# Optimization experiments

Hardware: AMD Instinct MI355X
Metric: run time of the kernel (lower is better)

The kernel has to match this reference:

```python
import jax, jax.numpy as jnp
import numpy as np

N = 100000
INC = 128
GRID = 256
S = 2  # scale s for voxel_to_aux coarse pooling


def _ln(x, g, b, eps=1e-6):
    m = jnp.mean(x, axis=-1, keepdims=True)
    v = jnp.var(x, axis=-1, keepdims=True)
    return (x - m) / jnp.sqrt(v + eps) * g + b


def setup_inputs() -> dict:
    rng = np.random.default_rng(0)
    lin = rng.choice(GRID ** 3, size=N, replace=False)
    x = (lin // (GRID * GRID)).astype(np.int64)
    y = ((lin // GRID) % GRID).astype(np.int64)
    z = (lin % GRID).astype(np.int64)
    coords = np.stack([x, y, z], axis=1).astype(np.int32)
    # sparse 3x3x3 neighbor table (pad index = N for missing neighbors)
    order = np.argsort(lin)
    lin_sorted = lin[order]
    nbr_idx = np.full((N, 27), N, dtype=np.int32)
    k = 0
    for dx in (-1, 0, 1):
        for dy in (-1, 0, 1):
            for dz in (-1, 0, 1):
                nx, ny, nz = x + dx, y + dy, z + dz
                valid = (nx >= 0) & (nx < GRID) & (ny >= 0) & (ny < GRID) & (nz >= 0) & (nz < GRID)
                nlin = (nx * GRID + ny) * GRID + nz
                pos = np.clip(np.searchsorted(lin_sorted, nlin), 0, N - 1)
                found = valid & (lin_sorted[pos] == nlin)
                nbr_idx[:, k] = np.where(found, order[pos].astype(np.int32), N)
                k += 1
    # voxel_to_aux: coarse voxel id at scale S; counts per coarse voxel
    G2 = GRID // S
    clin = ((x // S) * G2 + (y // S)) * G2 + (z // S)
    uniq, aux_idx, counts = np.unique(clin, return_inverse=True, return_counts=True)
    counts_v = counts[aux_idx].astype(np.float32)
    num_aux = int(len(uniq))

    key = jax.random.key(0)
    ks = jax.random.split(key, 6)
    sd = 1.0 / np.sqrt(INC)
    return {
        "F": jax.random.normal(ks[0], (N, INC), jnp.float32),
        "coords": jnp.asarray(coords),
        "nbr_idx": jnp.asarray(nbr_idx),
        "aux_idx": jnp.asarray(aux_idx.astype(np.int32)),
        "counts_v": jnp.asarray(counts_v),
        "num_aux": num_aux,
        "alpha": jnp.ones((1, INC), jnp.float32),
        "w_pos": jax.random.normal(ks[1], (INC, 3), jnp.float32) * (1.0 / np.sqrt(3.0)),
        "w_pre": jax.random.normal(ks[2], (INC, INC), jnp.float32) * sd,
        "g_pre": jnp.ones((INC,), jnp.float32),
        "b_pre": jnp.zeros((INC,), jnp.float32),
        "w_conv": jax.random.normal(ks[3], (27, INC, INC), jnp.float32) * (sd / np.sqrt(27.0)),
        "g_local": jnp.ones((INC,), jnp.float32),
        "b_local": jnp.zeros((INC,), jnp.float32),
        "g_norm": jnp.ones((INC,), jnp.float32),
        "b_norm": jnp.zeros((INC,), jnp.float32),
    }


def reference(F, coords, nbr_idx, aux_idx, counts_v, num_aux, alpha, w_pos, w_pre,
              g_pre, b_pre, w_conv, g_local, b_local, g_norm, b_norm):
    inc = F.shape[1]
    # pre_mix: Linear (no bias) + LayerNorm
    F_input = _ln(F @ w_pre.T, g_pre, b_pre)
    # local_mix: sparse 3x3x3 conv on ORIGINAL features via neighbor gather
    Fp = jnp.concatenate([F, jnp.zeros((1, inc), F.dtype)], axis=0)
    gathered = Fp[nbr_idx]                               # [N, 27, inc]
    local = jnp.einsum('nkc,kcd->nd', gathered, w_conv)  # [N, inc]
    # cos_x positional reweighting
    pos = (coords.astype(jnp.float32) @ w_pos.T) * alpha  # [N, inc]
    psin, pcos = jnp.sin(pos), jnp.cos(pos)
    cat = jnp.concatenate([F_input * pcos, F_input * psin, F_input * pos], axis=1)  # [N, 3*inc]
    # voxel_to_aux (sum pool per coarse voxel) + aux_to_voxel (mean broadcast back)
    aux = jax.ops.segment_sum(cat, aux_idx, num_segments=num_aux)
    vox = aux[aux_idx] / counts_v[:, None]
    new = (vox[:, :inc] * pcos + vox[:, inc:2 * inc] * psin
           + (vox[:, 2 * inc:] - F_input * pos))
    new = _ln(new, g_norm, b_norm)
    local = _ln(local, g_local, b_local)
    return jax.nn.relu(new + local)
```

## Files before the change

### kernel.cpp

```cpp
#include <hip/hip_runtime.h>
#include <hip/hip_bf16.h>
#include <stdint.h>

#define N_PTS 100000
#define INC 128
#define NSLOT 27
#define CAPP 8192

typedef float f32x4 __attribute__((ext_vector_type(4)));
typedef short bf16x8 __attribute__((ext_vector_type(8)));

static const size_t OFF_WP   = 0;
static const size_t SZ_WP    = (size_t)NSLOT * INC * INC * 2;
static const size_t OFF_WPRE = (OFF_WP + SZ_WP + 255) & ~(size_t)255;
static const size_t SZ_WPRE  = (size_t)INC * INC * 2;
static const size_t OFF_FIN  = (OFF_WPRE + SZ_WPRE + 255) & ~(size_t)255;
static const size_t SZ_FIN   = (size_t)N_PTS * INC * 2;
static const size_t OFF_LOC  = (OFF_FIN + SZ_FIN + 255) & ~(size_t)255;
static const size_t SZ_LOC   = (size_t)N_PTS * INC * 4;
static const size_t OFF_LOC2 = (OFF_LOC + SZ_LOC + 255) & ~(size_t)255;
static const size_t SZ_LOC2  = (size_t)N_PTS * INC * 4;
static const size_t OFF_CNT  = (OFF_LOC2 + SZ_LOC2 + 255) & ~(size_t)255;
static const size_t SZ_CNT   = 128;
static const size_t OFF_DST  = (OFF_CNT + SZ_CNT + 255) & ~(size_t)255;
static const size_t SZ_DST   = (size_t)26 * CAPP * 4;
static const size_t OFF_SRC  = (OFF_DST + SZ_DST + 255) & ~(size_t)255;
static const size_t SZ_SRC   = (size_t)26 * CAPP * 4;
static const size_t OFF_FLG  = (OFF_SRC + SZ_SRC + 255) & ~(size_t)255;
static const size_t SZ_FLG   = (size_t)N_PTS;
static const size_t OFF_NDL  = (OFF_FLG + SZ_FLG + 255) & ~(size_t)255;
static const size_t SZ_NDL   = (size_t)N_PTS * 4;

#define PREP_BLOCKS 1792
#define SCAN_BLOCKS 391
#define MT64 1563
#define PAIRB 256

__device__ __forceinline__ float compute_pos3(float w0, float w1, float w2, float a,
                                              float cx, float cy, float cz) {
    return (cx * w0 + cy * w1 + cz * w2) * a;
}

__device__ __forceinline__ bf16x8 ld_cvt8(const float* __restrict__ p) {
    const float4 u = *(const float4*)p;
    const float4 v = *(const float4*)(p + 4);
    bf16x8 r;
    __hip_bfloat16* h = (__hip_bfloat16*)&r;
    h[0] = __float2bfloat16(u.x); h[1] = __float2bfloat16(u.y);
    h[2] = __float2bfloat16(u.z); h[3] = __float2bfloat16(u.w);
    h[4] = __float2bfloat16(v.x); h[5] = __float2bfloat16(v.y);
    h[6] = __float2bfloat16(v.z); h[7] = __float2bfloat16(v.w);
    return r;
}

__global__ __launch_bounds__(256) void k_front(
        const float* __restrict__ w_pre, const float* __restrict__ w_conv,
        __hip_bfloat16* __restrict__ Wp, __hip_bfloat16* __restrict__ Wpre,
        const int* __restrict__ nbr_idx, const float* __restrict__ counts_v,
        int* __restrict__ cnt, int* __restrict__ dst, int* __restrict__ src,
        unsigned char* __restrict__ flg, int* __restrict__ ndl,
        float* __restrict__ loc2) {
    __shared__ unsigned long long s_msk[4][26];
    __shared__ unsigned long long s_ndm[4];
    __shared__ int s_base[26];
    __shared__ int s_nbase;

    const int tid = threadIdx.x;

    if (blockIdx.x < PREP_BLOCKS) {
        int i = blockIdx.x * 256 + tid;
        if (i < 16384) {
            int d = i >> 7, c = i & 127;
            int j = ((c >> 5) << 12) | ((d >> 4) << 9)
                  | (((((c >> 3) & 3) << 4) + (d & 15)) << 3) | (c & 7);
            Wpre[j] = __float2bfloat16(w_pre[i]);
        } else if (i < 16384 + NSLOT * 16384) {
            int t = i - 16384;
            int slot = t >> 14, rem = t & 16383;
            int c = rem >> 7, d = rem & 127;
            int j = (slot << 14) | ((c >> 5) << 12) | ((d >> 4) << 9)
                  | (((((c >> 3) & 3) << 4) + (d & 15)) << 3) | (c & 7);
            Wp[j] = __float2bfloat16(w_conv[t]);
        }
        return;
    }

    const int w = tid >> 6, lane = tid & 63;
    const int p = (blockIdx.x - PREP_BLOCKS) * 256 + tid;
    const bool vp = p < N_PTS;

    float cv = vp ? counts_v[p] : 0.f;
    bool multi = cv > 1.5f;

    const int* nb = nbr_idx + (size_t)p * NSLOT;
    int nbr_r[NSLOT];
#pragma unroll
    for (int k = 0; k < NSLOT; ++k) nbr_r[k] = vp ? nb[k] : N_PTS;

    bool hn = false;
#pragma unroll
    for (int k = 0; k < NSLOT; ++k) {
        if (k == 13) continue;
        bool valid = nbr_r[k] < N_PTS;
        hn = hn || valid;
        unsigned long long msk = __ballot(valid);
        int b = k < 13 ? k : k - 1;
        if (lane == 0) s_msk[w][b] = msk;
    }
    bool ndv = vp && (hn || multi);
    unsigned long long ndm = __ballot(ndv);
    if (lane == 0) s_ndm[w] = ndm;
    __syncthreads();

    if (tid < 26) {
        int tot = 0;
#pragma unroll
        for (int ww = 0; ww < 4; ++ww) tot += __popcll(s_msk[ww][tid]);
        s_base[tid] = tot ? atomicAdd(&cnt[tid], tot) : 0;
    } else if (tid == 32) {
        int tot = 0;
#pragma unroll
        for (int ww = 0; ww < 4; ++ww) tot += __popcll(s_ndm[ww]);
        s_nbase = tot ? atomicAdd(&cnt[26], tot) : 0;
    }
    __syncthreads();

#pragma unroll
    for (int k = 0; k < NSLOT; ++k) {
        if (k == 13) continue;
        int b = k < 13 ? k : k - 1;
        if (nbr_r[k] < N_PTS) {
            unsigned long long msk = s_msk[w][b];
            int pre = 0;
            for (int ww = 0; ww < w; ++ww) pre += __popcll(s_msk[ww][b]);
            int gi = s_base[b] + pre + __popcll(msk & ((1ull << lane) - 1ull));
            if (gi < CAPP) { dst[b * CAPP + gi] = p; src[b * CAPP + gi] = nbr_r[k]; }
        }
    }

    if (vp) flg[p] = (unsigned char)(ndv ? 1 : 0);
    if (ndv) {
        float4* row = (float4*)(loc2 + (size_t)p * INC);
#pragma unroll
        for (int i = 0; i < INC / 4; ++i) row[i] = make_float4(0.f, 0.f, 0.f, 0.f);
        unsigned long long m2 = s_ndm[w];
        int pre = 0;
        for (int ww = 0; ww < w; ++ww) pre += __popcll(s_ndm[ww]);
        ndl[s_nbase + pre + __popcll(m2 & ((1ull << lane) - 1ull))] = p;
    }
}

__global__ __launch_bounds__(256, 3) void k_main(
        const float* __restrict__ F, const __hip_bfloat16* __restrict__ Wpre,
        const __hip_bfloat16* __restrict__ Wp, const unsigned char* __restrict__ flg,
        const float* __restrict__ g_pre, const float* __restrict__ b_pre,
        const float* __restrict__ g_local, const float* __restrict__ b_local,
        const float* __restrict__ g_norm, const float* __restrict__ b_norm,
        const int* __restrict__ cnt, const int* __restrict__ dst,
        const int* __restrict__ src,
        __hip_bfloat16* __restrict__ F_input, float* __restrict__ loc,
        float* __restrict__ loc2, float* __restrict__ outp) {
    __shared__ __hip_bfloat16 s_bf[4][16 * 136];
    __shared__ float s_gp[INC], s_bp[INC], s_gl[INC], s_bl[INC], s_gn[INC], s_bn[INC];
    __shared__ int s_wre[27], s_cntb[26];

    const int tid = threadIdx.x, w = tid >> 6, lane = tid & 63;
    const int q = lane >> 4, l15 = lane & 15;

    if (blockIdx.x >= MT64) {
        const int pb = blockIdx.x - MT64;
        if (tid < 26) { int v = cnt[tid]; if (v > CAPP) v = CAPP; s_cntb[tid] = v; }
        __syncthreads();
        if (tid == 0) {
            int accw = 0; s_wre[0] = 0;
            for (int b = 0; b < 26; ++b) { accw += (s_cntb[b] + 15) >> 4; s_wre[b + 1] = accw; }
        }
        __syncthreads();
        const int W = s_wre[26];
#pragma unroll 1
        for (int wvi = pb * 4 + w; wvi < W; wvi += PAIRB * 4) {
            int b = 0;
            while (wvi >= s_wre[b + 1]) ++b;
            int base = (wvi - s_wre[b]) << 4;
            int nB = s_cntb[b];
            int slot = b < 13 ? b : b + 1;
            const int* srcb = src + b * CAPP;
            const int* dstb = dst + b * CAPP;
            int mrow = (base + l15 < nB) ? srcb[base + l15] : 0;
            const bf16x8* Bp = (const bf16x8*)Wp + (size_t)slot * 2048;

            f32x4 acc[8];
#pragma unroll
            for (int j = 0; j < 8; ++j) acc[j] = (f32x4){0.f, 0.f, 0.f, 0.f};
#pragma unroll
            for (int ks = 0; ks < 4; ++ks) {
                bf16x8 a2 = ld_cvt8(F + (size_t)mrow * INC + ks * 32 + q * 8);
#pragma unroll
                for (int j = 0; j < 8; ++j)
                    acc[j] = __builtin_amdgcn_mfma_f32_16x16x32_bf16(
                        a2, Bp[(ks * 8 + j) * 64 + lane], acc[j], 0, 0, 0);
            }
#pragma unroll
            for (int r = 0; r < 4; ++r) {
                int m = (q << 2) + r;
                int ri = base + m;
                if (ri < nB) {
                    int d = dstb[ri];
                    float* lp = loc2 + (size_t)d * INC + l15;
#pragma unroll
                    for (int j = 0; j < 8; ++j) atomicAdd(lp + (j << 4), acc[j][r]);
                }
            }
        }
        return;
    }

    const int p0 = blockIdx.x * 64;

    if (tid < INC) {
        s_gp[tid] = g_pre[tid];   s_bp[tid] = b_pre[tid];
        s_gl[tid] = g_local[tid]; s_bl[tid] = b_local[tid];
        s_gn[tid] = g_norm[tid];  s_bn[tid] = b_norm[tid];
    }
    __syncthreads();

    int grow = p0 + (w << 4) + l15;
    if (grow >= N_PTS) grow = N_PTS - 1;

    const float* A = F + (size_t)grow * INC + q * 8;

    unsigned int fe = *(const unsigned int*)(flg + p0 + (w << 4) + (q << 2));
    unsigned char fs0 = flg[p0 + (w << 4) + q];
    unsigned char fs1 = flg[p0 + (w << 4) + 4 + q];
    unsigned char fs2 = flg[p0 + (w << 4) + 8 + q];
    unsigned char fs3 = flg[p0 + (w << 4) + 12 + q];

    bf16x8 a[4];
#pragma unroll
    for (int ks = 0; ks < 4; ++ks) a[ks] = ld_cvt8(A + ks * 32);

    const bf16x8* BP = (const bf16x8*)Wpre;
    const bf16x8* BL = (const bf16x8*)Wp + (size_t)13 * 2048;
    f32x4 accP[8], accL[8];
#pragma unroll
    for (int j = 0; j < 8; ++j) {
        accP[j] = (f32x4){0.f, 0.f, 0.f, 0.f};
        accL[j] = (f32x4){0.f, 0.f, 0.f, 0.f};
    }
    bf16x8 bP[8], bL[8];
#pragma unroll
    for (int j = 0; j < 8; ++j) bP[j] = BP[j * 64 + lane];
#pragma unroll
    for (int ks = 0; ks < 4; ++ks) {
#pragma unroll
        for (int j = 0; j < 8; ++j) bL[j] = BL[(ks * 8 + j) * 64 + lane];
#pragma unroll
        for (int j = 0; j < 8; ++j)
            accP[j] = __builtin_amdgcn_mfma_f32_16x16x32_bf16(a[ks], bP[j], accP[j], 0, 0, 0);
        if (ks < 3) {
#pragma unroll
            for (int j = 0; j < 8; ++j) bP[j] = BP[((ks + 1) * 8 + j) * 64 + lane];
        }
#pragma unroll
        for (int j = 0; j < 8; ++j)
            accL[j] = __builtin_amdgcn_mfma_f32_16x16x32_bf16(a[ks], bL[j], accL[j], 0, 0, 0);
    }

    __hip_bfloat16* sb = s_bf[w];
#pragma unroll
    for (int r = 0; r < 4; ++r) {
        int ri = (q << 2) + r;
        int p = p0 + (w << 4) + ri;
        int fl = (p < N_PTS) ? (int)((fe >> (r * 8)) & 1) : 1;

        float s = 0.f, ss = 0.f;
#pragma unroll
        for (int j = 0; j < 8; ++j) { float v = accP[j][r]; s += v; ss += v * v; }
#pragma unroll
        for (int m = 1; m < 16; m <<= 1) { s += __shfl_xor(s, m); ss += __shfl_xor(ss, m); }
        float mean = s * (1.f / 128.f);
        float rstd = rsqrtf(ss * (1.f / 128.f) - mean * mean + 1e-6f);

        float fj[8], sN = 0.f, ssN = 0.f, sL = 0.f, ssL = 0.f;
#pragma unroll
        for (int j = 0; j < 8; ++j) {
            int c = (j << 4) + l15;
            float fi = (accP[j][r] - mean) * rstd * s_gp[c] + s_bp[c];
            __hip_bfloat16 fb = __float2bfloat16(fi);
            sb[ri * 136 + c] = fb;
            float f = __bfloat162float(fb);
            fj[j] = f; sN += f; ssN += f * f;
            float v = accL[j][r]; sL += v; ssL += v * v;
        }
#pragma unroll
        for (int m = 1; m < 16; m <<= 1) {
            sN += __shfl_xor(sN, m); ssN += __shfl_xor(ssN, m);
            sL += __shfl_xor(sL, m); ssL += __shfl_xor(ssL, m);
        }
        float meanN = sN * (1.f / 128.f);
        float rstdN = rsqrtf(ssN * (1.f / 128.f) - meanN * meanN + 1e-6f);
        float meanL = sL * (1.f / 128.f);
        float rstdL = rsqrtf(ssL * (1.f / 128.f) - meanL * meanL + 1e-6f);

        if (p < N_PTS) {
            float* dp = fl ? (loc + (size_t)p * INC) : (outp + (size_t)p * INC);
#pragma unroll
            for (int j = 0; j < 8; ++j) {
                int c = (j << 4) + l15;
                float lvj = accL[j][r];
                float nn = (fj[j] - meanN) * rstdN * s_gn[c] + s_bn[c];
                float ll = (lvj - meanL) * rstdL * s_gl[c] + s_bl[c];
                float o = nn + ll; o = o > 0.f ? o : 0.f;
                dp[c] = fl ? lvj : o;
            }
        }
    }

    unsigned char fsv[4] = {fs0, fs1, fs2, fs3};
#pragma unroll
    for (int t = 0; t < 4; ++t) {
        int row = (t << 2) + q;
        int p = p0 + (w << 4) + row;
        if (p < N_PTS && (fsv[t] & 1)) {
            bf16x8 v = *(const bf16x8*)&sb[row * 136 + l15 * 8];
            *(bf16x8*)(F_input + (size_t)p * INC + l15 * 8) = v;
        }
    }
}

__global__ __launch_bounds__(256) void k_final(
        const __hip_bfloat16* __restrict__ F_input, const float* __restrict__ loc,
        const float* __restrict__ loc2,
        const int* __restrict__ nbr_idx, const int* __restrict__ coords,
        const float* __restrict__ counts_v,
        const float* __restrict__ w_pos, const float* __restrict__ alpha,
        const float* __restrict__ g_local, const float* __restrict__ b_local,
        const float* __restrict__ g_norm, const float* __restrict__ b_norm,
        const int* __restrict__ cnt, const int* __restrict__ ndl,
        float* __restrict__ out) {
    const int tid = threadIdx.x, g = tid >> 4, l15 = tid & 15;
    const int c0 = l15 * 8;
    const int nd = cnt[26];
    if (blockIdx.x * 16 >= nd) return;

    float wpv[24], pa[8], gl[8], bl[8], gn[8], bn[8];
#pragma unroll
    for (int t = 0; t < 6; ++t) ((float4*)wpv)[t] = ((const float4*)(w_pos + c0 * 3))[t];
#pragma unroll
    for (int t = 0; t < 2; ++t) {
        ((float4*)pa)[t] = ((const float4*)(alpha   + c0))[t];
        ((float4*)gl)[t] = ((const float4*)(g_local + c0))[t];
        ((float4*)bl)[t] = ((const float4*)(b_local + c0))[t];
        ((float4*)gn)[t] = ((const float4*)(g_norm  + c0))[t];
        ((float4*)bn)[t] = ((const float4*)(b_norm  + c0))[t];
    }

    for (int base = blockIdx.x * 16; base < nd; base += gridDim.x * 16) {
        int idx = base + g;
        if (idx >= nd) continue;
        int p = ndl[idx];

        float lv[8], s = 0.f, ss = 0.f;
        float4 la0 = *(const float4*)(loc  + (size_t)p * INC + c0);
        float4 la1 = *(const float4*)(loc  + (size_t)p * INC + c0 + 4);
        float4 lb0 = *(const float4*)(loc2 + (size_t)p * INC + c0);
        float4 lb1 = *(const float4*)(loc2 + (size_t)p * INC + c0 + 4);
        lv[0] = la0.x + lb0.x; lv[1] = la0.y + lb0.y;
        lv[2] = la0.z + lb0.z; lv[3] = la0.w + lb0.w;
        lv[4] = la1.x + lb1.x; lv[5] = la1.y + lb1.y;
        lv[6] = la1.z + lb1.z; lv[7] = la1.w + lb1.w;
#pragma unroll
        for (int j = 0; j < 8; ++j) { s += lv[j]; ss += lv[j] * lv[j]; }
#pragma unroll
        for (int m = 1; m < 16; m <<= 1) { s += __shfl_xor(s, m); ss += __shfl_xor(ss, m); }
        float meanL = s * (1.f / 128.f);
        float rstdL = rsqrtf(ss * (1.f / 128.f) - meanL * meanL + 1e-6f);

        float cv = counts_v[p];
        bool multi = cv > 1.5f;
        int ix = coords[p * 3 + 0], iy = coords[p * 3 + 1], iz = coords[p * 3 + 2];
        float cx = (float)ix, cy = (float)iy, cz = (float)iz;

        bf16x8 fbv = *(const bf16x8*)(F_input + (size_t)p * INC + c0);

        float psO[8], snO[8], csO[8], fO[8];
#pragma unroll
        for (int j = 0; j < 8; ++j) {
            fO[j] = __bfloat162float(((__hip_bfloat16*)&fbv)[j]);
            psO[j] = compute_pos3(wpv[j * 3], wpv[j * 3 + 1], wpv[j * 3 + 2], pa[j], cx, cy, cz);
            snO[j] = __sinf(psO[j]); csO[j] = __cosf(psO[j]);
        }

        float v0[8], v1[8], v2[8];
        if (multi) {
            float invc = 1.f / cv;
            int ox = (ix & 1) ? -1 : 1, oy = (iy & 1) ? -1 : 1, oz = (iz & 1) ? -1 : 1;
            const int* nb = nbr_idx + (size_t)p * NSLOT;
            unsigned vmask = 1u;
            bf16x8 fmv8[8];
            fmv8[0] = fbv;
#pragma unroll
            for (int e = 1; e < 8; ++e) {
                int dx = (e & 4) ? ox : 0, dy = (e & 2) ? oy : 0, dz = (e & 1) ? oz : 0;
                int m = nb[(dx + 1) * 9 + (dy + 1) * 3 + (dz + 1)];
                bool ok = m < N_PTS;
                if (ok) vmask |= (1u << e);
                int mc = ok ? m : p;
                fmv8[e] = *(const bf16x8*)(F_input + (size_t)mc * INC + c0);
            }
#pragma unroll
            for (int j = 0; j < 8; ++j) { v0[j] = 0.f; v1[j] = 0.f; v2[j] = 0.f; }
#pragma unroll
            for (int e = 0; e < 8; ++e) {
                float wt = ((vmask >> e) & 1u) ? 1.f : 0.f;
                int dx = (e & 4) ? ox : 0, dy = (e & 2) ? oy : 0, dz = (e & 1) ? oz : 0;
                float mx = cx + (float)dx, my = cy + (float)dy, mz = cz + (float)dz;
#pragma unroll
                for (int j = 0; j < 8; ++j) {
                    float fm = wt * __bfloat162float(((__hip_bfloat16*)&fmv8[e])[j]);
                    float ps = compute_pos3(wpv[j * 3], wpv[j * 3 + 1], wpv[j * 3 + 2], pa[j],
                                            mx, my, mz);
                    v0[j] += fm * __cosf(ps);
                    v1[j] += fm * __sinf(ps);
                    v2[j] += fm * ps;
                }
            }
#pragma unroll
            for (int j = 0; j < 8; ++j) { v0[j] *= invc; v1[j] *= invc; v2[j] *= invc; }
        } else {
#pragma unroll
            for (int j = 0; j < 8; ++j) {
                v0[j] = fO[j] * csO[j]; v1[j] = fO[j] * snO[j]; v2[j] = fO[j] * psO[j];
            }
        }

        float nv[8], s2 = 0.f, ss2 = 0.f;
#pragma unroll
        for (int j = 0; j < 8; ++j) {
            float nw = v0[j] * csO[j] + v1[j] * snO[j] + v2[j] - fO[j] * psO[j];
            nv[j] = nw; s2 += nw; ss2 += nw * nw;
        }
#pragma unroll
        for (int m = 1; m < 16; m <<= 1) { s2 += __shfl_xor(s2, m); ss2 += __shfl_xor(ss2, m); }
        float meanN = s2 * (1.f / 128.f);
        float rstdN = rsqrtf(ss2 * (1.f / 128.f) - meanN * meanN + 1e-6f);
        float ov[8];
#pragma unroll
        for (int j = 0; j < 8; ++j) {
            float nn = (nv[j] - meanN) * rstdN * gn[j] + bn[j];
            float ll = (lv[j] - meanL) * rstdL * gl[j] + bl[j];
            float o = nn + ll;
            ov[j] = o > 0.f ? o : 0.f;
        }
        float4* op = (float4*)(out + (size_t)p * INC + c0);
        op[0] = ((float4*)ov)[0];
        op[1] = ((float4*)ov)[1];
    }
}

extern "C" void kernel_launch(void* const* d_in, const int* in_sizes, int n_in,
                              void* d_out, int out_size, void* d_ws, size_t ws_size,
                              hipStream_t stream) {
    (void)in_sizes; (void)n_in; (void)out_size; (void)ws_size;
    const float* F        = (const float*)d_in[0];
    const int*   coords   = (const int*)d_in[1];
    const int*   nbr      = (const int*)d_in[2];
    const float* counts_v = (const float*)d_in[4];
    const float* alpha    = (const float*)d_in[6];
    const float* w_pos    = (const float*)d_in[7];
    const float* w_pre    = (const float*)d_in[8];
    const float* g_pre    = (const float*)d_in[9];
    const float* b_pre    = (const float*)d_in[10];
    const float* w_conv   = (const float*)d_in[11];
    const float* g_local  = (const float*)d_in[12];
    const float* b_local  = (const float*)d_in[13];
    const float* g_norm   = (const float*)d_in[14];
    const float* b_norm   = (const float*)d_in[15];
    float* out = (float*)d_out;

    char* ws = (char*)d_ws;
    __hip_bfloat16* Wp      = (__hip_bfloat16*)(ws + OFF_WP);
    __hip_bfloat16* Wpre    = (__hip_bfloat16*)(ws + OFF_WPRE);
    __hip_bfloat16* F_input = (__hip_bfloat16*)(ws + OFF_FIN);
    float*          loc     = (float*)(ws + OFF_LOC);
    float*          loc2    = (float*)(ws + OFF_LOC2);
    int*            cnt     = (int*)(ws + OFF_CNT);
    int*            dstb    = (int*)(ws + OFF_DST);
    int*            srcb    = (int*)(ws + OFF_SRC);
    unsigned char*  flg     = (unsigned char*)(ws + OFF_FLG);
    int*            ndl     = (int*)(ws + OFF_NDL);

    hipMemsetAsync(cnt, 0, SZ_CNT, stream);
    k_front<<<PREP_BLOCKS + SCAN_BLOCKS, 256, 0, stream>>>(
        w_pre, w_conv, Wp, Wpre, nbr, counts_v, cnt, dstb, srcb, flg, ndl, loc2);
    k_main<<<MT64 + PAIRB, 256, 0, stream>>>(
        F, Wpre, Wp, flg, g_pre, b_pre, g_local, b_local, g_norm, b_norm,
        cnt, dstb, srcb, F_input, loc, loc2, out);
    k_final<<<1024, 256, 0, stream>>>(F_input, loc, loc2, nbr, coords, counts_v,
                                      w_pos, alpha, g_local, b_local, g_norm, b_norm,
                                      cnt, ndl, out);
}
```

Measured before the change: 209.3 us.

## Drop separate loc buffer, atomically accumulate center-tap into loc2, simplify singleton path

Removes the separate `loc` workspace. The center-tap conv result for flagged points is now added atomically into `loc2` instead of being written to its own buffer and summed back in k_final. Zeroing of `loc2` rows becomes a wave-cooperative float2 store per flagged row instead of per-thread float4 loops. k_final now skips the sin/cos/pos computation for singleton voxels, where the positional terms cancel, and computes it only in the multi-point branch. Together these cut memory traffic and trig work, at the cost of atomics on the center tap and a possible race ordering with the pair-block atomics.

After: 201.5 us. 1.04x faster.

```diff
diff --git a/kernel.cpp b/kernel.cpp
--- a/kernel.cpp
+++ b/kernel.cpp
@@ -16,9 +16,7 @@
 static const size_t SZ_WPRE  = (size_t)INC * INC * 2;
 static const size_t OFF_FIN  = (OFF_WPRE + SZ_WPRE + 255) & ~(size_t)255;
 static const size_t SZ_FIN   = (size_t)N_PTS * INC * 2;
-static const size_t OFF_LOC  = (OFF_FIN + SZ_FIN + 255) & ~(size_t)255;
-static const size_t SZ_LOC   = (size_t)N_PTS * INC * 4;
-static const size_t OFF_LOC2 = (OFF_LOC + SZ_LOC + 255) & ~(size_t)255;
+static const size_t OFF_LOC2 = (OFF_FIN + SZ_FIN + 255) & ~(size_t)255;
 static const size_t SZ_LOC2  = (size_t)N_PTS * INC * 4;
 static const size_t OFF_CNT  = (OFF_LOC2 + SZ_LOC2 + 255) & ~(size_t)255;
 static const size_t SZ_CNT   = 128;
@@ -139,14 +137,18 @@
     }
 
     if (vp) flg[p] = (unsigned char)(ndv ? 1 : 0);
+    unsigned long long m2 = s_ndm[w];
     if (ndv) {
-        float4* row = (float4*)(loc2 + (size_t)p * INC);
-#pragma unroll
-        for (int i = 0; i < INC / 4; ++i) row[i] = make_float4(0.f, 0.f, 0.f, 0.f);
-        unsigned long long m2 = s_ndm[w];
         int pre = 0;
         for (int ww = 0; ww < w; ++ww) pre += __popcll(s_ndm[ww]);
         ndl[s_nbase + pre + __popcll(m2 & ((1ull << lane) - 1ull))] = p;
+    }
+    int wave_p0 = (blockIdx.x - PREP_BLOCKS) * 256 + (w << 6);
+    unsigned long long mz = m2;
+    while (mz) {
+        int e = __ffsll((unsigned long long)mz) - 1;
+        mz &= mz - 1;
+        *(float2*)(loc2 + (size_t)(wave_p0 + e) * INC + (lane << 1)) = make_float2(0.f, 0.f);
     }
 }
 
@@ -158,8 +160,8 @@
         const float* __restrict__ g_norm, const float* __restrict__ b_norm,
         const int* __restrict__ cnt, const int* __restrict__ dst,
         const int* __restrict__ src,
-        __hip_bfloat16* __restrict__ F_input, float* __restrict__ loc,
-        float* __restrict__ loc2, float* __restrict__ outp) {
+        __hip_bfloat16* __restrict__ F_input, float* __restrict__ loc2,
+        float* __restrict__ outp) {
     __shared__ __hip_bfloat16 s_bf[4][16 * 136];
     __shared__ float s_gp[INC], s_bp[INC], s_gl[INC], s_bl[INC], s_gn[INC], s_bn[INC];
     __shared__ int s_wre[27], s_cntb[26];
@@ -229,11 +231,9 @@
 
     const float* A = F + (size_t)grow * INC + q * 8;
 
-    unsigned int fe = *(const unsigned int*)(flg + p0 + (w << 4) + (q << 2));
-    unsigned char fs0 = flg[p0 + (w << 4) + q];
-    unsigned char fs1 = flg[p0 + (w << 4) + 4 + q];
-    unsigned char fs2 = flg[p0 + (w << 4) + 8 + q];
-    unsigned char fs3 = flg[p0 + (w << 4) + 12 + q];
+    const uint32_t* fwp = (const uint32_t*)(flg + p0 + (w << 4));
+    uint32_t fq0 = fwp[0], fq1 = fwp[1], fq2 = fwp[2], fq3 = fwp[3];
+    uint32_t fqv[4] = {fq0, fq1, fq2, fq3};
 
     bf16x8 a[4];
 #pragma unroll
@@ -271,7 +271,7 @@
     for (int r = 0; r < 4; ++r) {
         int ri = (q << 2) + r;
         int p = p0 + (w << 4) + ri;
-        int fl = (p < N_PTS) ? (int)((fe >> (r * 8)) & 1) : 1;
+        int fl = (p < N_PTS) ? (int)((fqv[q] >> (r * 8)) & 1u) : 1;
 
         float s = 0.f, ss = 0.f;
 #pragma unroll
@@ -303,25 +303,29 @@
         float rstdL = rsqrtf(ssL * (1.f / 128.f) - meanL * meanL + 1e-6f);
 
         if (p < N_PTS) {
-            float* dp = fl ? (loc + (size_t)p * INC) : (outp + (size_t)p * INC);
-#pragma unroll
-            for (int j = 0; j < 8; ++j) {
-                int c = (j << 4) + l15;
-                float lvj = accL[j][r];
-                float nn = (fj[j] - meanN) * rstdN * s_gn[c] + s_bn[c];
-                float ll = (lvj - meanL) * rstdL * s_gl[c] + s_bl[c];
-                float o = nn + ll; o = o > 0.f ? o : 0.f;
-                dp[c] = fl ? lvj : o;
-            }
-        }
-    }
-
-    unsigned char fsv[4] = {fs0, fs1, fs2, fs3};
+            if (fl) {
+                float* lp = loc2 + (size_t)p * INC;
+#pragma unroll
+                for (int j = 0; j < 8; ++j) atomicAdd(lp + (j << 4) + l15, accL[j][r]);
+            } else {
+                float* op2 = outp + (size_t)p * INC;
+#pragma unroll
+                for (int j = 0; j < 8; ++j) {
+                    int c = (j << 4) + l15;
+                    float nn = (fj[j] - meanN) * rstdN * s_gn[c] + s_bn[c];
+                    float ll = (accL[j][r] - meanL) * rstdL * s_gl[c] + s_bl[c];
+                    float o = nn + ll;
+                    op2[c] = o > 0.f ? o : 0.f;
+                }
+            }
+        }
+    }
+
 #pragma unroll
     for (int t = 0; t < 4; ++t) {
         int row = (t << 2) + q;
         int p = p0 + (w << 4) + row;
-        if (p < N_PTS && (fsv[t] & 1)) {
+        if (p < N_PTS && ((fqv[t] >> (q * 8)) & 1u)) {
             bf16x8 v = *(const bf16x8*)&sb[row * 136 + l15 * 8];
             *(bf16x8*)(F_input + (size_t)p * INC + l15 * 8) = v;
         }
@@ -329,8 +333,7 @@
 }
 
 __global__ __launch_bounds__(256) void k_final(
-        const __hip_bfloat16* __restrict__ F_input, const float* __restrict__ loc,
-        const float* __restrict__ loc2,
+        const __hip_bfloat16* __restrict__ F_input, const float* __restrict__ loc2,
         const int* __restrict__ nbr_idx, const int* __restrict__ coords,
         const float* __restrict__ counts_v,
         const float* __restrict__ w_pos, const float* __restrict__ alpha,
@@ -343,12 +346,9 @@
     const int nd = cnt[26];
     if (blockIdx.x * 16 >= nd) return;
 
-    float wpv[24], pa[8], gl[8], bl[8], gn[8], bn[8];
-#pragma unroll
-    for (int t = 0; t < 6; ++t) ((float4*)wpv)[t] = ((const float4*)(w_pos + c0 * 3))[t];
+    float gl[8], bl[8], gn[8], bn[8];
 #pragma unroll
     for (int t = 0; t < 2; ++t) {
-        ((float4*)pa)[t] = ((const float4*)(alpha   + c0))[t];
         ((float4*)gl)[t] = ((const float4*)(g_local + c0))[t];
         ((float4*)bl)[t] = ((const float4*)(b_local + c0))[t];
         ((float4*)gn)[t] = ((const float4*)(g_norm  + c0))[t];
@@ -361,14 +361,8 @@
         int p = ndl[idx];
 
         float lv[8], s = 0.f, ss = 0.f;
-        float4 la0 = *(const float4*)(loc  + (size_t)p * INC + c0);
-        float4 la1 = *(const float4*)(loc  + (size_t)p * INC + c0 + 4);
-        float4 lb0 = *(const float4*)(loc2 + (size_t)p * INC + c0);
-        float4 lb1 = *(const float4*)(loc2 + (size_t)p * INC + c0 + 4);
-        lv[0] = la0.x + lb0.x; lv[1] = la0.y + lb0.y;
-        lv[2] = la0.z + lb0.z; lv[3] = la0.w + lb0.w;
-        lv[4] = la1.x + lb1.x; lv[5] = la1.y + lb1.y;
-        lv[6] = la1.z + lb1.z; lv[7] = la1.w + lb1.w;
+        ((float4*)lv)[0] = *(const float4*)(loc2 + (size_t)p * INC + c0);
+        ((float4*)lv)[1] = *(const float4*)(loc2 + (size_t)p * INC + c0 + 4);
 #pragma unroll
         for (int j = 0; j < 8; ++j) { s += lv[j]; ss += lv[j] * lv[j]; }
 #pragma unroll
@@ -376,26 +370,26 @@
         float meanL = s * (1.f / 128.f);
         float rstdL = rsqrtf(ss * (1.f / 128.f) - meanL * meanL + 1e-6f);
 
+        bf16x8 fbv = *(const bf16x8*)(F_input + (size_t)p * INC + c0);
+        float fO[8];
+#pragma unroll
+        for (int j = 0; j < 8; ++j) fO[j] = __bfloat162float(((__hip_bfloat16*)&fbv)[j]);
+
         float cv = counts_v[p];
-        bool multi = cv > 1.5f;
-        int ix = coords[p * 3 + 0], iy = coords[p * 3 + 1], iz = coords[p * 3 + 2];
-        float cx = (float)ix, cy = (float)iy, cz = (float)iz;
-
-        bf16x8 fbv = *(const bf16x8*)(F_input + (size_t)p * INC + c0);
-
-        float psO[8], snO[8], csO[8], fO[8];
-#pragma unroll
-        for (int j = 0; j < 8; ++j) {
-            fO[j] = __bfloat162float(((__hip_bfloat16*)&fbv)[j]);
-            psO[j] = compute_pos3(wpv[j * 3], wpv[j * 3 + 1], wpv[j * 3 + 2], pa[j], cx, cy, cz);
-            snO[j] = __sinf(psO[j]); csO[j] = __cosf(psO[j]);
-        }
-
-        float v0[8], v1[8], v2[8];
-        if (multi) {
+        float nv[8];
+        if (cv > 1.5f) {
             float invc = 1.f / cv;
+            int ix = coords[p * 3 + 0], iy = coords[p * 3 + 1], iz = coords[p * 3 + 2];
+            float cx = (float)ix, cy = (float)iy, cz = (float)iz;
             int ox = (ix & 1) ? -1 : 1, oy = (iy & 1) ? -1 : 1, oz = (iz & 1) ? -1 : 1;
             const int* nb = nbr_idx + (size_t)p * NSLOT;
+
+            float wpv[24], pa[8];
+#pragma unroll
+            for (int t = 0; t < 6; ++t) ((float4*)wpv)[t] = ((const float4*)(w_pos + c0 * 3))[t];
+#pragma unroll
+            for (int t = 0; t < 2; ++t) ((float4*)pa)[t] = ((const float4*)(alpha + c0))[t];
+
             unsigned vmask = 1u;
             bf16x8 fmv8[8];
             fmv8[0] = fbv;
@@ -408,6 +402,7 @@
                 int mc = ok ? m : p;
                 fmv8[e] = *(const bf16x8*)(F_input + (size_t)mc * INC + c0);
             }
+            float v0[8], v1[8], v2[8];
 #pragma unroll
             for (int j = 0; j < 8; ++j) { v0[j] = 0.f; v1[j] = 0.f; v2[j] = 0.f; }
 #pragma unroll
@@ -426,20 +421,20 @@
                 }
             }
 #pragma unroll
-            for (int j = 0; j < 8; ++j) { v0[j] *= invc; v1[j] *= invc; v2[j] *= invc; }
+            for (int j = 0; j < 8; ++j) {
+                float ps = compute_pos3(wpv[j * 3], wpv[j * 3 + 1], wpv[j * 3 + 2], pa[j],
+                                        cx, cy, cz);
+                float sn = __sinf(ps), cs = __cosf(ps);
+                nv[j] = v0[j] * invc * cs + v1[j] * invc * sn + v2[j] * invc - fO[j] * ps;
+            }
         } else {
 #pragma unroll
-            for (int j = 0; j < 8; ++j) {
-                v0[j] = fO[j] * csO[j]; v1[j] = fO[j] * snO[j]; v2[j] = fO[j] * psO[j];
-            }
-        }
-
-        float nv[8], s2 = 0.f, ss2 = 0.f;
-#pragma unroll
-        for (int j = 0; j < 8; ++j) {
-            float nw = v0[j] * csO[j] + v1[j] * snO[j] + v2[j] - fO[j] * psO[j];
-            nv[j] = nw; s2 += nw; ss2 += nw * nw;
-        }
+            for (int j = 0; j < 8; ++j) nv[j] = fO[j];
+        }
+
+        float s2 = 0.f, ss2 = 0.f;
+#pragma unroll
+        for (int j = 0; j < 8; ++j) { s2 += nv[j]; ss2 += nv[j] * nv[j]; }
 #pragma unroll
         for (int m = 1; m < 16; m <<= 1) { s2 += __shfl_xor(s2, m); ss2 += __shfl_xor(ss2, m); }
         float meanN = s2 * (1.f / 128.f);
@@ -482,7 +477,6 @@
     __hip_bfloat16* Wp      = (__hip_bfloat16*)(ws + OFF_WP);
     __hip_bfloat16* Wpre    = (__hip_bfloat16*)(ws + OFF_WPRE);
     __hip_bfloat16* F_input = (__hip_bfloat16*)(ws + OFF_FIN);
-    float*          loc     = (float*)(ws + OFF_LOC);
     float*          loc2    = (float*)(ws + OFF_LOC2);
     int*            cnt     = (int*)(ws + OFF_CNT);
     int*            dstb    = (int*)(ws + OFF_DST);
@@ -495,8 +489,8 @@
         w_pre, w_conv, Wp, Wpre, nbr, counts_v, cnt, dstb, srcb, flg, ndl, loc2);
     k_main<<<MT64 + PAIRB, 256, 0, stream>>>(
         F, Wpre, Wp, flg, g_pre, b_pre, g_local, b_local, g_norm, b_norm,
-        cnt, dstb, srcb, F_input, loc, loc2, out);
-    k_final<<<1024, 256, 0, stream>>>(F_input, loc, loc2, nbr, coords, counts_v,
+        cnt, dstb, srcb, F_input, loc2, out);
+    k_final<<<1024, 256, 0, stream>>>(F_input, loc2, nbr, coords, counts_v,
                                       w_pos, alpha, g_local, b_local, g_norm, b_norm,
                                       cnt, ndl, out);
 }
```
